# Optimization experiments

Hardware: AMD Instinct MI355X
Metric: run time of the kernel (lower is better)

Reference implementation:

```python
import jax, jax.numpy as jnp
import numpy as np

B, CIN, K, H, W = 8, 256, 128, 112, 112


def setup_inputs() -> dict:
    key = jax.random.key(0)
    k1, k2, k3, k4 = jax.random.split(key, 4)
    return {
        "x": jax.random.normal(k1, (B, CIN, H, W), jnp.float32),
        "linComb": jax.random.uniform(k2, (K, CIN), dtype=jnp.float32),
        "geoParams": jax.random.uniform(k3, (K, 2, 3), dtype=jnp.float32),
        "boxParams": jax.random.uniform(k4, (K, 2, 3), dtype=jnp.float32),
    }


def _affine_sample(img, theta):
    """F.affine_grid + F.grid_sample (bilinear, zeros padding, align_corners=False).
    img: [B, K, H, W] (one feature channel per geometric channel k)
    theta: [K, 2, 3] affine params, shared across batch.
    """
    Bn, Kn, Hn, Wn = img.shape
    # normalized output coords (align_corners=False pixel centers)
    xs = (2.0 * jnp.arange(Wn, dtype=img.dtype) + 1.0) / Wn - 1.0
    ys = (2.0 * jnp.arange(Hn, dtype=img.dtype) + 1.0) / Hn - 1.0
    gxv, gyv = jnp.meshgrid(xs, ys)  # [H, W]
    coords = jnp.stack([gxv, gyv, jnp.ones_like(gxv)], axis=-1)  # [H, W, 3]
    grid = jnp.einsum('kij,hwj->khwi', theta, coords)  # [K, H, W, 2] (x, y)
    # unnormalize to input pixel space
    ix = ((grid[..., 0] + 1.0) * Wn - 1.0) * 0.5
    iy = ((grid[..., 1] + 1.0) * Hn - 1.0) * 0.5
    x0 = jnp.floor(ix)
    y0 = jnp.floor(iy)
    wx1 = ix - x0
    wx0 = 1.0 - wx1
    wy1 = iy - y0
    wy0 = 1.0 - wy1
    imgf = img.reshape(Bn, Kn, Hn * Wn)

    def gather(xc, yc, w):
        valid = (xc >= 0) & (xc <= Wn - 1) & (yc >= 0) & (yc <= Hn - 1)
        xi = jnp.clip(xc, 0, Wn - 1).astype(jnp.int32)
        yi = jnp.clip(yc, 0, Hn - 1).astype(jnp.int32)
        idx = (yi * Wn + xi).reshape(Kn, Hn * Wn)
        vals = jnp.take_along_axis(
            imgf, jnp.broadcast_to(idx[None], (Bn, Kn, Hn * Wn)), axis=2
        ).reshape(Bn, Kn, Hn, Wn)
        return vals * (w * valid.astype(img.dtype))[None]

    out = (gather(x0, y0, wx0 * wy0)
           + gather(x0 + 1.0, y0, wx1 * wy0)
           + gather(x0, y0 + 1.0, wx0 * wy1)
           + gather(x0 + 1.0, y0 + 1.0, wx1 * wy1))
    return out


def reference(x, linComb, geoParams, boxParams):
    # channel-weighted sum: (x.unsqueeze(1) * linComb).sum(dim=2) == 1x1-conv GEMM
    comb = jnp.einsum('bchw,kc->bkhw', x, linComb)  # [B, K, H, W]
    box = _affine_sample(jnp.ones_like(comb), boxParams)
    warped = _affine_sample(comb, geoParams)
    finalPred = warped * box
    return (finalPred, warped, box)
```

## Files before the change

### kernel.cpp

```cpp
#include <hip/hip_runtime.h>
#include <hip/hip_bf16.h>

namespace {
constexpr int Bn = 8, Cn = 256, Kn = 128, Hn = 112, Wn = 112;
constexpr int Pn = Hn * Wn;
constexpr long long NOUT = (long long)Bn * Kn * Pn;

typedef __attribute__((ext_vector_type(8))) short bf16x8;
typedef __attribute__((ext_vector_type(4))) float f32x4;

__device__ inline unsigned short f2bf(float f) {
  __hip_bfloat16 h = __float2bfloat16(f);
  return __builtin_bit_cast(unsigned short, h);
}
__device__ inline unsigned int pack2bf(float a, float b) {
  return (unsigned int)f2bf(a) | ((unsigned int)f2bf(b) << 16);
}
__device__ inline float bf2f(unsigned short u) {
  return __bfloat162float(__builtin_bit_cast(__hip_bfloat16, u));
}
}

__global__ __launch_bounds__(256) void prep_lcQ(const float* __restrict__ lc,
                                                unsigned int* __restrict__ lcQ) {
  int idx = blockIdx.x * 256 + threadIdx.x;
  int r = idx & 3;
  int l15 = (idx >> 2) & 15;
  int l4 = (idx >> 6) & 3;
  int ks = (idx >> 8) & 7;
  int s = idx >> 11;
  int c2 = s * 16 + l4 * 4 + r;
  int k = ks * 16 + l15;
  lcQ[idx] = pack2bf(lc[k * Cn + 2 * c2], lc[k * Cn + 2 * c2 + 1]);
}

__global__ __launch_bounds__(256) void gemm_mfma(const float* __restrict__ x,
                                                 const uint4* __restrict__ lcQ4,
                                                 unsigned short* __restrict__ combh) {
  const int tid = threadIdx.x;
  const int wid = tid >> 6;
  const int lane = tid & 63;
  const int l15 = lane & 15, l4 = lane >> 4;
  const int b = blockIdx.x / 98;
  const int p0 = (blockIdx.x % 98) * 128 + wid * 32;
  const float* xb = x + (size_t)b * Cn * Pn;

  f32x4 acc[8][2];
#pragma unroll
  for (int ks = 0; ks < 8; ++ks)
#pragma unroll
    for (int ps = 0; ps < 2; ++ps) acc[ks][ps] = (f32x4)(0.f);

#pragma unroll 2
  for (int s = 0; s < 8; ++s) {
    unsigned int a[2][4];
#pragma unroll
    for (int ps = 0; ps < 2; ++ps) {
      const float* src = xb + (size_t)(32 * s + l4 * 8) * Pn + (p0 + ps * 16 + l15);
      float v[8];
#pragma unroll
      for (int j = 0; j < 8; ++j) v[j] = src[(size_t)j * Pn];
#pragma unroll
      for (int r = 0; r < 4; ++r) a[ps][r] = pack2bf(v[2 * r], v[2 * r + 1]);
    }
#pragma unroll
    for (int ks = 0; ks < 8; ++ks) {
      uint4 bq = lcQ4[((s * 8 + ks) * 4 + l4) * 16 + l15];
      union { uint4 q; bf16x8 v; } bu;
      bu.q = bq;
#pragma unroll
      for (int ps = 0; ps < 2; ++ps) {
        union { unsigned int u[4]; bf16x8 v; } au;
        au.u[0] = a[ps][0]; au.u[1] = a[ps][1]; au.u[2] = a[ps][2]; au.u[3] = a[ps][3];
        acc[ks][ps] = __builtin_amdgcn_mfma_f32_16x16x32_bf16(au.v, bu.v, acc[ks][ps], 0, 0, 0);
      }
    }
  }

#pragma unroll
  for (int ks = 0; ks < 8; ++ks) {
    const size_t krow = ((size_t)b * Kn + ks * 16 + l15) * Pn;
#pragma unroll
    for (int ps = 0; ps < 2; ++ps) {
      const int p = p0 + ps * 16 + l4 * 4;
      uint2 st;
      st.x = pack2bf(acc[ks][ps][0], acc[ks][ps][1]);
      st.y = pack2bf(acc[ks][ps][2], acc[ks][ps][3]);
      *reinterpret_cast<uint2*>(combh + krow + p) = st;
    }
  }
}

template <int FUSE>
__global__ __launch_bounds__(256) void sample_all(const unsigned short* __restrict__ comb,
                                                  const float* __restrict__ geo,
                                                  const float* __restrict__ boxp,
                                                  float* __restrict__ outF,
                                                  float* __restrict__ outW,
                                                  float* __restrict__ outB) {
  const int k = blockIdx.y;
  const int p = blockIdx.x * 256 + threadIdx.x;
  const int h = p / Wn;
  const int w = p - h * Wn;
  const float xn = (2.f * w + 1.f) / (float)Wn - 1.f;
  const float yn = (2.f * h + 1.f) / (float)Hn - 1.f;

  const float* g = geo + k * 6;
  const float* t = boxp + k * 6;

  float ix = ((g[0] * xn + g[1] * yn + g[2] + 1.f) * Wn - 1.f) * 0.5f;
  float iy = ((g[3] * xn + g[4] * yn + g[5] + 1.f) * Hn - 1.f) * 0.5f;
  float x0f = floorf(ix), y0f = floorf(iy);
  float wx1 = ix - x0f, wx0 = 1.f - wx1;
  float wy1 = iy - y0f, wy0 = 1.f - wy1;
  float vx0 = (x0f >= 0.f && x0f <= (float)(Wn - 1)) ? 1.f : 0.f;
  float vx1 = (x0f + 1.f >= 0.f && x0f + 1.f <= (float)(Wn - 1)) ? 1.f : 0.f;
  float vy0 = (y0f >= 0.f && y0f <= (float)(Hn - 1)) ? 1.f : 0.f;
  float vy1 = (y0f + 1.f >= 0.f && y0f + 1.f <= (float)(Hn - 1)) ? 1.f : 0.f;
  int x0i = (int)fminf(fmaxf(x0f, 0.f), (float)(Wn - 1));
  int x1i = (int)fminf(fmaxf(x0f + 1.f, 0.f), (float)(Wn - 1));
  int y0i = (int)fminf(fmaxf(y0f, 0.f), (float)(Hn - 1));
  int y1i = (int)fminf(fmaxf(y0f + 1.f, 0.f), (float)(Hn - 1));
  float w00 = wx0 * wy0 * vx0 * vy0;
  float w01 = wx1 * wy0 * vx1 * vy0;
  float w10 = wx0 * wy1 * vx0 * vy1;
  float w11 = wx1 * wy1 * vx1 * vy1;
  int i00 = y0i * Wn + x0i, i01 = y0i * Wn + x1i;
  int i10 = y1i * Wn + x0i, i11 = y1i * Wn + x1i;

  float bix = ((t[0] * xn + t[1] * yn + t[2] + 1.f) * Wn - 1.f) * 0.5f;
  float biy = ((t[3] * xn + t[4] * yn + t[5] + 1.f) * Hn - 1.f) * 0.5f;
  float bx0 = floorf(bix), by0 = floorf(biy);
  float bwx1 = bix - bx0, bwx0 = 1.f - bwx1;
  float bwy1 = biy - by0, bwy0 = 1.f - bwy1;
  float bvx0 = (bx0 >= 0.f && bx0 <= (float)(Wn - 1)) ? 1.f : 0.f;
  float bvx1 = (bx0 + 1.f >= 0.f && bx0 + 1.f <= (float)(Wn - 1)) ? 1.f : 0.f;
  float bvy0 = (by0 >= 0.f && by0 <= (float)(Hn - 1)) ? 1.f : 0.f;
  float bvy1 = (by0 + 1.f >= 0.f && by0 + 1.f <= (float)(Hn - 1)) ? 1.f : 0.f;
  float bv = bwx0 * bwy0 * bvx0 * bvy0 + bwx1 * bwy0 * bvx1 * bvy0 +
             bwx0 * bwy1 * bvx0 * bvy1 + bwx1 * bwy1 * bvx1 * bvy1;

#pragma unroll
  for (int b = 0; b < Bn; ++b) {
    const unsigned short* cp = comb + ((size_t)b * Kn + k) * Pn;
    float v = w00 * bf2f(cp[i00]) + w01 * bf2f(cp[i01]) +
              w10 * bf2f(cp[i10]) + w11 * bf2f(cp[i11]);
    size_t o = ((size_t)b * Kn + k) * Pn + p;
    __builtin_nontemporal_store(v, &outW[o]);
    __builtin_nontemporal_store(bv, &outB[o]);
    if (FUSE) __builtin_nontemporal_store(v * bv, &outF[o]);
  }
}

__global__ __launch_bounds__(256) void mul_fw(const float* __restrict__ w,
                                              const float* __restrict__ bx,
                                              float* __restrict__ f) {
  const long long n4 = NOUT / 4;
  const f32x4* w4 = reinterpret_cast<const f32x4*>(w);
  const f32x4* b4 = reinterpret_cast<const f32x4*>(bx);
  f32x4* f4 = reinterpret_cast<f32x4*>(f);
  for (long long i = blockIdx.x * 256LL + threadIdx.x; i < n4;
       i += (long long)gridDim.x * 256LL) {
    f32x4 r = w4[i] * b4[i];
    __builtin_nontemporal_store(r, &f4[i]);
  }
}

extern "C" void kernel_launch(void* const* d_in, const int* in_sizes, int n_in,
                              void* d_out, int out_size, void* d_ws, size_t ws_size,
                              hipStream_t stream) {
  (void)in_sizes; (void)n_in; (void)out_size;
  const float* x = (const float*)d_in[0];
  const float* lc = (const float*)d_in[1];
  const float* geo = (const float*)d_in[2];
  const float* boxp = (const float*)d_in[3];
  float* outF = (float*)d_out;
  float* outW = outF + NOUT;
  float* outB = outW + NOUT;

  unsigned int* lcQ = (unsigned int*)outB;

  const size_t comb_bytes = (size_t)NOUT * sizeof(unsigned short);
  const bool use_ws = ws_size >= comb_bytes;
  unsigned short* combh = use_ws ? (unsigned short*)d_ws : (unsigned short*)outF;

  prep_lcQ<<<64, 256, 0, stream>>>(lc, lcQ);
  gemm_mfma<<<Bn * (Pn / 128), 256, 0, stream>>>(x, (const uint4*)lcQ, combh);
  if (use_ws) {
    sample_all<1><<<dim3(Pn / 256, Kn), 256, 0, stream>>>(combh, geo, boxp, outF, outW, outB);
  } else {
    sample_all<0><<<dim3(Pn / 256, Kn), 256, 0, stream>>>(combh, geo, boxp, outF, outW, outB);
    mul_fw<<<2048, 256, 0, stream>>>(outW, outB, outF);
  }
}
```

Before: 295.6 us.

## Stage each comb image in LDS for sampling and shrink GEMM tiles

The sampler now uses one block per (batch, channel) image. Each block copies that bf16 comb image into shared memory, then serves all four bilinear taps from LDS instead of scattered global gathers, and always writes the fused final output. Affine coordinates are now recomputed once per batch rather than shared across the 8 batches. The GEMM tile is halved to 64 pixels per block, giving twice as many blocks with fewer accumulators each. The fallback path for a small workspace, including the separate multiply kernel, is removed, so if comb ever lived in outF, blocks would race between reading comb and writing outF.

```diff
diff --git a/kernel.cpp b/kernel.cpp
--- a/kernel.cpp
+++ b/kernel.cpp
@@ -41,128 +41,109 @@
   const int wid = tid >> 6;
   const int lane = tid & 63;
   const int l15 = lane & 15, l4 = lane >> 4;
-  const int b = blockIdx.x / 98;
-  const int p0 = (blockIdx.x % 98) * 128 + wid * 32;
+  const int b = blockIdx.x / 196;
+  const int p0 = (blockIdx.x % 196) * 64 + wid * 16;
   const float* xb = x + (size_t)b * Cn * Pn;
 
-  f32x4 acc[8][2];
+  f32x4 acc[8];
 #pragma unroll
-  for (int ks = 0; ks < 8; ++ks)
-#pragma unroll
-    for (int ps = 0; ps < 2; ++ps) acc[ks][ps] = (f32x4)(0.f);
+  for (int ks = 0; ks < 8; ++ks) acc[ks] = (f32x4)(0.f);
 
 #pragma unroll 2
   for (int s = 0; s < 8; ++s) {
-    unsigned int a[2][4];
+    const float* src = xb + (size_t)(32 * s + l4 * 8) * Pn + (p0 + l15);
+    float v[8];
 #pragma unroll
-    for (int ps = 0; ps < 2; ++ps) {
-      const float* src = xb + (size_t)(32 * s + l4 * 8) * Pn + (p0 + ps * 16 + l15);
-      float v[8];
+    for (int j = 0; j < 8; ++j) v[j] = src[(size_t)j * Pn];
+    union { unsigned int u[4]; bf16x8 vv; } au;
 #pragma unroll
-      for (int j = 0; j < 8; ++j) v[j] = src[(size_t)j * Pn];
-#pragma unroll
-      for (int r = 0; r < 4; ++r) a[ps][r] = pack2bf(v[2 * r], v[2 * r + 1]);
-    }
+    for (int r = 0; r < 4; ++r) au.u[r] = pack2bf(v[2 * r], v[2 * r + 1]);
 #pragma unroll
     for (int ks = 0; ks < 8; ++ks) {
-      uint4 bq = lcQ4[((s * 8 + ks) * 4 + l4) * 16 + l15];
-      union { uint4 q; bf16x8 v; } bu;
-      bu.q = bq;
-#pragma unroll
-      for (int ps = 0; ps < 2; ++ps) {
-        union { unsigned int u[4]; bf16x8 v; } au;
-        au.u[0] = a[ps][0]; au.u[1] = a[ps][1]; au.u[2] = a[ps][2]; au.u[3] = a[ps][3];
-        acc[ks][ps] = __builtin_amdgcn_mfma_f32_16x16x32_bf16(au.v, bu.v, acc[ks][ps], 0, 0, 0);
-      }
+      union { uint4 q; bf16x8 vv; } bu;
+      bu.q = lcQ4[((s * 8 + ks) * 4 + l4) * 16 + l15];
+      acc[ks] = __builtin_amdgcn_mfma_f32_16x16x32_bf16(au.vv, bu.vv, acc[ks], 0, 0, 0);
     }
   }
 
 #pragma unroll
   for (int ks = 0; ks < 8; ++ks) {
-    const size_t krow = ((size_t)b * Kn + ks * 16 + l15) * Pn;
-#pragma unroll
-    for (int ps = 0; ps < 2; ++ps) {
-      const int p = p0 + ps * 16 + l4 * 4;
-      uint2 st;
-      st.x = pack2bf(acc[ks][ps][0], acc[ks][ps][1]);
-      st.y = pack2bf(acc[ks][ps][2], acc[ks][ps][3]);
-      *reinterpret_cast<uint2*>(combh + krow + p) = st;
-    }
+    const size_t o = ((size_t)b * Kn + ks * 16 + l15) * Pn + p0 + l4 * 4;
+    uint2 st;
+    st.x = pack2bf(acc[ks][0], acc[ks][1]);
+    st.y = pack2bf(acc[ks][2], acc[ks][3]);
+    *reinterpret_cast<uint2*>(combh + o) = st;
   }
 }
 
-template <int FUSE>
-__global__ __launch_bounds__(256) void sample_all(const unsigned short* __restrict__ comb,
+__global__ __launch_bounds__(256) void sample_lds(const unsigned short* __restrict__ comb,
                                                   const float* __restrict__ geo,
                                                   const float* __restrict__ boxp,
                                                   float* __restrict__ outF,
                                                   float* __restrict__ outW,
                                                   float* __restrict__ outB) {
-  const int k = blockIdx.y;
-  const int p = blockIdx.x * 256 + threadIdx.x;
-  const int h = p / Wn;
-  const int w = p - h * Wn;
-  const float xn = (2.f * w + 1.f) / (float)Wn - 1.f;
-  const float yn = (2.f * h + 1.f) / (float)Hn - 1.f;
+  __shared__ __align__(16) unsigned short img[Pn];
+  const int bx = blockIdx.x;
+  const int k = bx & 127;
+  const int tid = threadIdx.x;
+
+  {
+    const uint4* src = reinterpret_cast<const uint4*>(comb + (size_t)bx * Pn);
+    uint4* dst = reinterpret_cast<uint4*>(img);
+    for (int i = tid; i < Pn / 8; i += 256) dst[i] = src[i];
+  }
+  __syncthreads();
 
   const float* g = geo + k * 6;
   const float* t = boxp + k * 6;
+  const float g0 = g[0], g1 = g[1], g2 = g[2], g3 = g[3], g4 = g[4], g5 = g[5];
+  const float t0 = t[0], t1 = t[1], t2 = t[2], t3 = t[3], t4 = t[4], t5 = t[5];
+  const size_t obase = (size_t)bx * Pn;
 
-  float ix = ((g[0] * xn + g[1] * yn + g[2] + 1.f) * Wn - 1.f) * 0.5f;
-  float iy = ((g[3] * xn + g[4] * yn + g[5] + 1.f) * Hn - 1.f) * 0.5f;
-  float x0f = floorf(ix), y0f = floorf(iy);
-  float wx1 = ix - x0f, wx0 = 1.f - wx1;
-  float wy1 = iy - y0f, wy0 = 1.f - wy1;
-  float vx0 = (x0f >= 0.f && x0f <= (float)(Wn - 1)) ? 1.f : 0.f;
-  float vx1 = (x0f + 1.f >= 0.f && x0f + 1.f <= (float)(Wn - 1)) ? 1.f : 0.f;
-  float vy0 = (y0f >= 0.f && y0f <= (float)(Hn - 1)) ? 1.f : 0.f;
-  float vy1 = (y0f + 1.f >= 0.f && y0f + 1.f <= (float)(Hn - 1)) ? 1.f : 0.f;
-  int x0i = (int)fminf(fmaxf(x0f, 0.f), (float)(Wn - 1));
-  int x1i = (int)fminf(fmaxf(x0f + 1.f, 0.f), (float)(Wn - 1));
-  int y0i = (int)fminf(fmaxf(y0f, 0.f), (float)(Hn - 1));
-  int y1i = (int)fminf(fmaxf(y0f + 1.f, 0.f), (float)(Hn - 1));
-  float w00 = wx0 * wy0 * vx0 * vy0;
-  float w01 = wx1 * wy0 * vx1 * vy0;
-  float w10 = wx0 * wy1 * vx0 * vy1;
-  float w11 = wx1 * wy1 * vx1 * vy1;
-  int i00 = y0i * Wn + x0i, i01 = y0i * Wn + x1i;
-  int i10 = y1i * Wn + x0i, i11 = y1i * Wn + x1i;
+  for (int pp = tid; pp < Pn; pp += 256) {
+    const int h = pp / Wn;
+    const int w = pp - h * Wn;
+    const float xn = (2.f * w + 1.f) / (float)Wn - 1.f;
+    const float yn = (2.f * h + 1.f) / (float)Hn - 1.f;
 
-  float bix = ((t[0] * xn + t[1] * yn + t[2] + 1.f) * Wn - 1.f) * 0.5f;
-  float biy = ((t[3] * xn + t[4] * yn + t[5] + 1.f) * Hn - 1.f) * 0.5f;
-  float bx0 = floorf(bix), by0 = floorf(biy);
-  float bwx1 = bix - bx0, bwx0 = 1.f - bwx1;
-  float bwy1 = biy - by0, bwy0 = 1.f - bwy1;
-  float bvx0 = (bx0 >= 0.f && bx0 <= (float)(Wn - 1)) ? 1.f : 0.f;
-  float bvx1 = (bx0 + 1.f >= 0.f && bx0 + 1.f <= (float)(Wn - 1)) ? 1.f : 0.f;
-  float bvy0 = (by0 >= 0.f && by0 <= (float)(Hn - 1)) ? 1.f : 0.f;
-  float bvy1 = (by0 + 1.f >= 0.f && by0 + 1.f <= (float)(Hn - 1)) ? 1.f : 0.f;
-  float bv = bwx0 * bwy0 * bvx0 * bvy0 + bwx1 * bwy0 * bvx1 * bvy0 +
-             bwx0 * bwy1 * bvx0 * bvy1 + bwx1 * bwy1 * bvx1 * bvy1;
+    float ix = ((g0 * xn + g1 * yn + g2 + 1.f) * Wn - 1.f) * 0.5f;
+    float iy = ((g3 * xn + g4 * yn + g5 + 1.f) * Hn - 1.f) * 0.5f;
+    float x0f = floorf(ix), y0f = floorf(iy);
+    float wx1 = ix - x0f, wx0 = 1.f - wx1;
+    float wy1 = iy - y0f, wy0 = 1.f - wy1;
+    float vx0 = (x0f >= 0.f && x0f <= (float)(Wn - 1)) ? 1.f : 0.f;
+    float vx1 = (x0f + 1.f >= 0.f && x0f + 1.f <= (float)(Wn - 1)) ? 1.f : 0.f;
+    float vy0 = (y0f >= 0.f && y0f <= (float)(Hn - 1)) ? 1.f : 0.f;
+    float vy1 = (y0f + 1.f >= 0.f && y0f + 1.f <= (float)(Hn - 1)) ? 1.f : 0.f;
+    int x0i = (int)fminf(fmaxf(x0f, 0.f), (float)(Wn - 1));
+    int x1i = (int)fminf(fmaxf(x0f + 1.f, 0.f), (float)(Wn - 1));
+    int y0i = (int)fminf(fmaxf(y0f, 0.f), (float)(Hn - 1));
+    int y1i = (int)fminf(fmaxf(y0f + 1.f, 0.f), (float)(Hn - 1));
+    float w00 = wx0 * wy0 * vx0 * vy0;
+    float w01 = wx1 * wy0 * vx1 * vy0;
+    float w10 = wx0 * wy1 * vx0 * vy1;
+    float w11 = wx1 * wy1 * vx1 * vy1;
+    int i00 = y0i * Wn + x0i, i01 = y0i * Wn + x1i;
+    int i10 = y1i * Wn + x0i, i11 = y1i * Wn + x1i;
 
-#pragma unroll
-  for (int b = 0; b < Bn; ++b) {
-    const unsigned short* cp = comb + ((size_t)b * Kn + k) * Pn;
-    float v = w00 * bf2f(cp[i00]) + w01 * bf2f(cp[i01]) +
-              w10 * bf2f(cp[i10]) + w11 * bf2f(cp[i11]);
-    size_t o = ((size_t)b * Kn + k) * Pn + p;
+    float bix = ((t0 * xn + t1 * yn + t2 + 1.f) * Wn - 1.f) * 0.5f;
+    float biy = ((t3 * xn + t4 * yn + t5 + 1.f) * Hn - 1.f) * 0.5f;
+    float bx0 = floorf(bix), by0 = floorf(biy);
+    float bwx1 = bix - bx0, bwx0 = 1.f - bwx1;
+    float bwy1 = biy - by0, bwy0 = 1.f - bwy1;
+    float bvx0 = (bx0 >= 0.f && bx0 <= (float)(Wn - 1)) ? 1.f : 0.f;
+    float bvx1 = (bx0 + 1.f >= 0.f && bx0 + 1.f <= (float)(Wn - 1)) ? 1.f : 0.f;
+    float bvy0 = (by0 >= 0.f && by0 <= (float)(Hn - 1)) ? 1.f : 0.f;
+    float bvy1 = (by0 + 1.f >= 0.f && by0 + 1.f <= (float)(Hn - 1)) ? 1.f : 0.f;
+    float bv = bwx0 * bwy0 * bvx0 * bvy0 + bwx1 * bwy0 * bvx1 * bvy0 +
+               bwx0 * bwy1 * bvx0 * bvy1 + bwx1 * bwy1 * bvx1 * bvy1;
+
+    float v = w00 * bf2f(img[i00]) + w01 * bf2f(img[i01]) +
+              w10 * bf2f(img[i10]) + w11 * bf2f(img[i11]);
+    const size_t o = obase + pp;
     __builtin_nontemporal_store(v, &outW[o]);
     __builtin_nontemporal_store(bv, &outB[o]);
-    if (FUSE) __builtin_nontemporal_store(v * bv, &outF[o]);
-  }
-}
-
-__global__ __launch_bounds__(256) void mul_fw(const float* __restrict__ w,
-                                              const float* __restrict__ bx,
-                                              float* __restrict__ f) {
-  const long long n4 = NOUT / 4;
-  const f32x4* w4 = reinterpret_cast<const f32x4*>(w);
-  const f32x4* b4 = reinterpret_cast<const f32x4*>(bx);
-  f32x4* f4 = reinterpret_cast<f32x4*>(f);
-  for (long long i = blockIdx.x * 256LL + threadIdx.x; i < n4;
-       i += (long long)gridDim.x * 256LL) {
-    f32x4 r = w4[i] * b4[i];
-    __builtin_nontemporal_store(r, &f4[i]);
+    __builtin_nontemporal_store(v * bv, &outF[o]);
   }
 }
 
@@ -185,11 +166,6 @@
   unsigned short* combh = use_ws ? (unsigned short*)d_ws : (unsigned short*)outF;
 
   prep_lcQ<<<64, 256, 0, stream>>>(lc, lcQ);
-  gemm_mfma<<<Bn * (Pn / 128), 256, 0, stream>>>(x, (const uint4*)lcQ, combh);
-  if (use_ws) {
-    sample_all<1><<<dim3(Pn / 256, Kn), 256, 0, stream>>>(combh, geo, boxp, outF, outW, outB);
-  } else {
-    sample_all<0><<<dim3(Pn / 256, Kn), 256, 0, stream>>>(combh, geo, boxp, outF, outW, outB);
-    mul_fw<<<2048, 256, 0, stream>>>(outW, outB, outF);
-  }
+  gemm_mfma<<<Bn * (Pn / 64), 256, 0, stream>>>(x, (const uint4*)lcQ, combh);
+  sample_lds<<<Bn * Kn, 256, 0, stream>>>(combh, geo, boxp, outF, outW, outB);
 }
```

Result: faster. 278.6 us (-5.8%).
